# Optimization experiments

Measured on AMD Instinct MI355X. Metric: run time of the kernel, lower is better.

The kernel has to match this reference:

```python
import jax, jax.numpy as jnp
import numpy as np

DIM, H, W, DEPTH = 256, 64, 64, 4
D_STATE, DT_RANK, D_CONV = 8, 16, 4
G, AGENTS = 8, 4

PKEYS = ['ln_w','ln_b','in_proj_w','conv_w','conv_b','x_proj_w','dt_proj_w','dt_proj_b',
         'A_log','A_b_log','D','out_proj_w','mn_w','mn_b']


def layernorm(x, w, b, eps=1e-5):
    mu = jnp.mean(x, -1, keepdims=True)
    var = jnp.var(x, -1, keepdims=True)
    return (x - mu) * jax.lax.rsqrt(var + eps) * w + b


def causal_conv1d(x, w, b):
    # x: (g, d, L); w: (d, k) depthwise causal conv (pad left k-1)
    k = w.shape[-1]
    xp = jnp.pad(x, ((0, 0), (0, 0), (k - 1, 0)))
    y = jax.lax.conv_general_dilated(xp, w[:, None, :], (1,), 'VALID',
                                     dimension_numbers=('NCH', 'OIH', 'NCH'),
                                     feature_group_count=w.shape[0])
    return y + b[None, :, None]


def selective_scan(u, delta, A, B, C, Dp, z):
    # u, delta, z: (g, d, L); B, C: (g, n, L); A: (d, n); Dp: (d,)
    dT = jnp.moveaxis(delta, -1, 0)
    BT = jnp.moveaxis(B, -1, 0)
    CT = jnp.moveaxis(C, -1, 0)
    uT = jnp.moveaxis(u, -1, 0)
    h0 = jnp.zeros(u.shape[:2] + (A.shape[-1],), u.dtype)  # (g, d, n)

    def step(h, inp):
        d_t, B_t, C_t, u_t = inp  # (g,d),(g,n),(g,n),(g,d)
        h = jnp.exp(d_t[..., None] * A) * h + (d_t * u_t)[..., None] * B_t[:, None, :]
        return h, jnp.einsum('gdn,gn->gd', h, C_t)

    _, ys = jax.lax.scan(step, h0, (dT, BT, CT, uT))
    y = jnp.moveaxis(ys, 0, -1) + Dp[None, :, None] * u
    return y * jax.nn.silu(z)


def ssm_dir(xdl, zdl, p, A):
    # one scan direction of mamba_inner_fn_no_out_proj; xdl, zdl: (g, d, L)
    xc = jax.nn.silu(causal_conv1d(xdl, p['conv_w'], p['conv_b']))
    x_dbl = jnp.einsum('gdl,ed->gel', xc, p['x_proj_w'])  # e = dt_rank + 2n
    dt, B, C = jnp.split(x_dbl, [DT_RANK, DT_RANK + D_STATE], axis=1)
    delta = jax.nn.softplus(jnp.einsum('grl,dr->gdl', dt, p['dt_proj_w'])
                            + p['dt_proj_b'][None, :, None])
    return selective_scan(xc, delta, A, B, C, p['D'], zdl)


def single_mamba_block(x, p):
    # x: (g, L, c)  -- LayerNorm + bidirectional Mamba (bimamba v1) + residual
    skip = x
    xn = layernorm(x, p['ln_w'], p['ln_b'])
    xz = jnp.einsum('glc,ec->gle', xn, p['in_proj_w'])  # (g, L, 2d), no bias
    xx, z = jnp.split(xz, 2, axis=-1)
    xdl = jnp.swapaxes(xx, 1, 2)
    zdl = jnp.swapaxes(z, 1, 2)
    y_f = ssm_dir(xdl, zdl, p, -jnp.exp(p['A_log']))
    y_b = jnp.flip(ssm_dir(jnp.flip(xdl, -1), jnp.flip(zdl, -1), p, -jnp.exp(p['A_b_log'])), -1)
    y = 0.5 * (y_f + y_b)  # if_devide_out=True
    out = jnp.einsum('gdl,od->glo', y, p['out_proj_w'])  # no bias
    out = layernorm(out, p['mn_w'], p['mn_b'])  # use_norm=True
    return out + skip


def _forward(data, plist, record_len):
    b, c, h, w = data.shape
    rl = np.asarray(record_len)
    seg = jnp.asarray(np.repeat(np.arange(rl.shape[0]), rl))
    means = jax.ops.segment_sum(data, seg, num_segments=rl.shape[0]) \
        / jnp.asarray(rl, data.dtype)[:, None, None, None]
    x = means.reshape(rl.shape[0], c, h * w).transpose(0, 2, 1)  # (G, L, C)
    for i in range(DEPTH):
        p = {k: v[i] for k, v in zip(PKEYS, plist)}
        x = single_mamba_block(x, p)
    return x.transpose(0, 2, 1).reshape(rl.shape[0], c, h, w)


def setup_inputs() -> dict:
    key = jax.random.key(0)
    ks = jax.random.split(key, 8)
    nrm = lambda k, shape, sc: jax.random.normal(k, shape, jnp.float32) * sc
    Alog = jnp.zeros((DEPTH, DIM, D_STATE), jnp.float32) \
        + jnp.log(jnp.arange(1, D_STATE + 1, dtype=jnp.float32))
    return {
        'data': jax.random.normal(ks[0], (G * AGENTS, DIM, H, W), jnp.float32),
        'ln_w': jnp.ones((DEPTH, DIM)), 'ln_b': jnp.zeros((DEPTH, DIM)),
        'in_proj_w': nrm(ks[1], (DEPTH, 2 * DIM, DIM), 0.02),
        'conv_w': nrm(ks[2], (DEPTH, DIM, D_CONV), 0.3),
        'conv_b': jnp.zeros((DEPTH, DIM)),
        'x_proj_w': nrm(ks[3], (DEPTH, DT_RANK + 2 * D_STATE, DIM), 0.02),
        'dt_proj_w': nrm(ks[4], (DEPTH, DIM, DT_RANK), 0.1),
        'dt_proj_b': jnp.full((DEPTH, DIM), float(np.log(np.expm1(0.01))), jnp.float32),
        'A_log': Alog, 'A_b_log': Alog,
        'D': jnp.ones((DEPTH, DIM)),
        'out_proj_w': nrm(ks[5], (DEPTH, DIM, DIM), 0.02),
        'mn_w': jnp.ones((DEPTH, DIM)), 'mn_b': jnp.zeros((DEPTH, DIM)),
        'record_len': jnp.full((G,), AGENTS, dtype=jnp.int32),
    }


def reference(data, ln_w, ln_b, in_proj_w, conv_w, conv_b, x_proj_w, dt_proj_w, dt_proj_b,
              A_log, A_b_log, D, out_proj_w, mn_w, mn_b, record_len):
    plist = [ln_w, ln_b, in_proj_w, conv_w, conv_b, x_proj_w, dt_proj_w, dt_proj_b,
             A_log, A_b_log, D, out_proj_w, mn_w, mn_b]
    return _forward(data, plist, record_len)
```

## Files before the change

### kernel.cpp

```cpp
#include <hip/hip_runtime.h>
#include <hip/hip_bf16.h>
#include <cstdint>
#include <cstddef>

typedef unsigned short u16;
typedef unsigned int   u32;

typedef short s16x8 __attribute__((ext_vector_type(8)));
typedef float f32x4 __attribute__((ext_vector_type(4)));

__device__ __forceinline__ float b2f(u16 u){ u32 x = ((u32)u)<<16; float f; __builtin_memcpy(&f,&x,4); return f; }
__device__ __forceinline__ u16  f2b(float f){ u32 x; __builtin_memcpy(&x,&f,4); u32 r = x + 0x7FFFu + ((x>>16)&1u); return (u16)(r>>16); }

__device__ __forceinline__ void unpack8(uint4 v, float* o){
  o[0]=b2f((u16)v.x); o[1]=b2f((u16)(v.x>>16));
  o[2]=b2f((u16)v.y); o[3]=b2f((u16)(v.y>>16));
  o[4]=b2f((u16)v.z); o[5]=b2f((u16)(v.z>>16));
  o[6]=b2f((u16)v.w); o[7]=b2f((u16)(v.w>>16));
}

__device__ __forceinline__ void gl_lds16(const u16* g, u16* l){
  __builtin_amdgcn_global_load_lds((const __attribute__((address_space(1))) u32*)g,
                                   (__attribute__((address_space(3))) u32*)l, 16, 0, 0);
}

__global__ void k_detect(const u16* __restrict__ lnw, int* __restrict__ flag){
  if (threadIdx.x==0 && blockIdx.x==0) *flag = (lnw[0] == 0x3F80) ? 1 : 0;
}

struct CvtTable { const void* src[14]; u16* dst[14]; int n[14]; };
__global__ void k_cvt(CvtTable t, const int* __restrict__ flag){
  int ti = blockIdx.y;
  int n = t.n[ti];
  int isbf = *flag;
  const u16*  sb = (const u16*)t.src[ti];
  const float* sf = (const float*)t.src[ti];
  u16* d = t.dst[ti];
  for (int i = blockIdx.x*256 + threadIdx.x; i < n; i += gridDim.x*256)
    d[i] = isbf ? sb[i] : f2b(sf[i]);
}

__global__ void k_mean(const void* __restrict__ data, const int* __restrict__ rl,
                       float* __restrict__ x, const int* __restrict__ flag){
  __shared__ float tile[32][129];
  int isbf = *flag;
  const u16*  db = (const u16*)data;
  const float* df_ = (const float*)data;
  int g = blockIdx.z, c0 = blockIdx.y*32, l0 = blockIdx.x*128;
  int tid = threadIdx.x;
  int off=0; for(int i=0;i<g;i++) off += rl[i];
  int cnt = rl[g];
  float inv = 1.0f/(float)cnt;
  for(int it=0; it<16; ++it){
    int idx = it*256 + tid;
    int ci = idx>>7, lj = idx&127;
    float acc = 0.f;
    for(int b=0;b<cnt;b++){
      size_t gi = ((size_t)(off+b)*256 + (c0+ci)) * 4096 + (l0+lj);
      acc += isbf ? b2f(db[gi]) : df_[gi];
    }
    tile[ci][lj] = acc*inv;
  }
  __syncthreads();
  for(int it=0; it<16; ++it){
    int idx = it*256 + tid;
    int lj = idx>>5, ci = idx&31;
    x[ ((size_t)g*4096 + (l0+lj))*256 + (c0+ci) ] = tile[ci][lj];
  }
}

__global__ void k_prep(const u16* __restrict__ dtp, const u16* __restrict__ xpw, u16* __restrict__ bcomb){
  int layer = blockIdx.y, row = blockIdx.x, c = threadIdx.x;
  u16 out;
  if (row < 256){
    float acc = 0.f;
    #pragma unroll
    for(int r=0;r<16;r++)
      acc += b2f(dtp[(size_t)layer*4096 + row*16 + r]) * b2f(xpw[(size_t)layer*8192 + r*256 + c]);
    out = f2b(acc);
  } else if (row < 272){
    out = xpw[(size_t)layer*8192 + (16 + row - 256)*256 + c];
  } else {
    out = 0;
  }
  bcomb[((size_t)layer*384 + row)*256 + c] = out;
}

__global__ void k_ln1(const float* __restrict__ x, u16* __restrict__ xnh, u16* __restrict__ xnl,
                      const u16* __restrict__ w, const u16* __restrict__ b, int layer){
  int wid = threadIdx.x>>6, lane = threadIdx.x&63;
  int row = blockIdx.x*4 + wid;
  const float* xr = x + (size_t)row*256;
  float4 v = *(const float4*)(xr + lane*4);
  float s = v.x+v.y+v.z+v.w;
  float q = v.x*v.x+v.y*v.y+v.z*v.z+v.w*v.w;
  for(int o=32;o;o>>=1){ s += __shfl_xor(s,o); q += __shfl_xor(q,o); }
  float mu = s*(1.f/256.f);
  float var = q*(1.f/256.f) - mu*mu;
  float rs = rsqrtf(var + 1e-5f);
  const u16* wp = w + layer*256 + lane*4;
  const u16* bp = b + layer*256 + lane*4;
  float vv[4] = {v.x,v.y,v.z,v.w};
  u16 h4[4], l4[4];
  #pragma unroll
  for(int k2=0;k2<4;k2++){
    float xv = (vv[k2]-mu)*rs*b2f(wp[k2]) + b2f(bp[k2]);
    h4[k2] = f2b(xv);
    l4[k2] = f2b(xv - b2f(h4[k2]));
  }
  uint2 oh; oh.x = (u32)h4[0] | ((u32)h4[1]<<16); oh.y = (u32)h4[2] | ((u32)h4[3]<<16);
  uint2 ol; ol.x = (u32)l4[0] | ((u32)l4[1]<<16); ol.y = (u32)l4[2] | ((u32)l4[3]<<16);
  *(uint2*)(xnh + (size_t)row*256 + lane*4) = oh;
  *(uint2*)(xnl + (size_t)row*256 + lane*4) = ol;
}

template<int MODE>
__global__ __launch_bounds__(256)
void k_gemm(const u16* __restrict__ A, const u16* __restrict__ Alo,
            const u16* __restrict__ B,
            u16* __restrict__ C0, float* __restrict__ C0f, int ldC,
            const u16* __restrict__ bias, u16* __restrict__ C1){
  __shared__ u16 As[128*64];
  __shared__ u16 Bs[128*64];
  __shared__ u16 Asl[(MODE==0)?(128*64):16];
  int tid = threadIdx.x, wid = tid>>6, lane = tid&63;
  int m0 = blockIdx.x*128, n0 = blockIdx.y*128;
  f32x4 acc[4][4];
  #pragma unroll
  for(int i=0;i<4;i++)
    #pragma unroll
    for(int j=0;j<4;j++) acc[i][j] = (f32x4){0.f,0.f,0.f,0.f};
  int lrow  = lane>>3;
  int scol  = ((lane&7) ^ lrow) * 8;
  int rm = (wid&1)*64, cn = (wid>>1)*64;
  for(int k0=0;k0<256;k0+=64){
    #pragma unroll
    for(int it=0; it<4; ++it){
      int chunk = wid*4 + it;
      int row = chunk*8 + lrow;
      gl_lds16(A + (size_t)(m0+row)*256 + k0 + scol, As + chunk*512 + lane*8);
      if (MODE==0)
        gl_lds16(Alo + (size_t)(m0+row)*256 + k0 + scol, Asl + chunk*512 + lane*8);
      gl_lds16(B + (size_t)(n0+row)*256 + k0 + scol, Bs + chunk*512 + lane*8);
    }
    __syncthreads();
    #pragma unroll
    for(int kk=0;kk<2;kk++){
      s16x8 af[4], afl[4], bfr[4];
      #pragma unroll
      for(int i=0;i<4;i++){
        int ar = rm + i*16 + (lane&15);
        int ap = (kk*4 + (lane>>4)) ^ (ar&7);
        af[i]  = *(const s16x8*)(As + ar*64 + ap*8);
        if (MODE==0) afl[i] = *(const s16x8*)(Asl + ar*64 + ap*8);
        int br = cn + i*16 + (lane&15);
        int bp = (kk*4 + (lane>>4)) ^ (br&7);
        bfr[i] = *(const s16x8*)(Bs + br*64 + bp*8);
      }
      #pragma unroll
      for(int i=0;i<4;i++)
        #pragma unroll
        for(int j=0;j<4;j++){
          acc[i][j] = __builtin_amdgcn_mfma_f32_16x16x32_bf16(af[i], bfr[j], acc[i][j], 0,0,0);
          if (MODE==0)
            acc[i][j] = __builtin_amdgcn_mfma_f32_16x16x32_bf16(afl[i], bfr[j], acc[i][j], 0,0,0);
        }
    }
    __syncthreads();
  }
  #pragma unroll
  for(int i=0;i<4;i++){
    #pragma unroll
    for(int j=0;j<4;j++){
      int n  = n0 + cn + j*16 + (lane&15);
      int mB = m0 + rm + i*16 + ((lane>>4)<<2);
      #pragma unroll
      for(int r=0;r<4;r++){
        float val = acc[i][j][r];
        int m = mB + r;
        if (MODE==0){
          C0f[(size_t)m*ldC + n] = val;
        } else {
          if (n < 256){
            float v2 = val + b2f(bias[n]);
            float sp = (v2 > 15.f) ? v2 : __logf(1.f + __expf(v2));
            C0[(size_t)m*256 + n] = f2b(sp);
          } else if (n < 272){
            C1[(size_t)m*16 + (n-256)] = f2b(val);
          }
        }
      }
    }
  }
}

__global__ void k_conv(const float* __restrict__ xzf, const u16* __restrict__ cw,
                       const u16* __restrict__ cb, u16* __restrict__ xcf, u16* __restrict__ xcb_, int layer){
  int l0 = blockIdx.x*32, g = blockIdx.y, d = threadIdx.x;
  float w[4];
  #pragma unroll
  for(int j=0;j<4;j++) w[j] = b2f(cw[(size_t)layer*1024 + d*4 + j]);
  float bb = b2f(cb[layer*256 + d]);
  float xv[38];
  #pragma unroll
  for(int t=0;t<38;t++){
    int lp = l0 - 3 + t;
    xv[t] = (lp>=0 && lp<4096) ? xzf[((size_t)g*4096 + lp)*512 + d] : 0.f;
  }
  #pragma unroll
  for(int i=0;i<32;i++){
    float af = bb, ab = bb;
    #pragma unroll
    for(int j=0;j<4;j++){ af += w[j]*xv[i+j]; ab += w[j]*xv[i+6-j]; }
    af = af / (1.f + __expf(-af));
    ab = ab / (1.f + __expf(-ab));
    size_t o = ((size_t)g*4096 + (l0+i))*256 + d;
    xcf[o]  = f2b(af);
    xcb_[o] = f2b(ab);
  }
}

__global__ __launch_bounds__(256)
void k_scan1(const u16* __restrict__ df, const u16* __restrict__ db,
             const u16* __restrict__ uf, const u16* __restrict__ ub,
             const u16* __restrict__ bcf, const u16* __restrict__ bcb,
             const u16* __restrict__ Alog, const u16* __restrict__ Ablog,
             float* __restrict__ abuf, float* __restrict__ bbuf, int layer){
  int c = blockIdx.x, g = blockIdx.y, dir = blockIdx.z, d = threadIdx.x;
  const u16* dl = dir ? db : df;
  const u16* uu = dir ? ub : uf;
  const u16* bc = dir ? bcb : bcf;
  const u16* Al = dir ? Ablog : Alog;
  float An[8], h[8], ap[8];
  #pragma unroll
  for(int n=0;n<8;n++){
    An[n] = -__expf(b2f(Al[(size_t)layer*2048 + d*8 + n]));
    h[n] = 0.f; ap[n] = 1.f;
  }
  #pragma unroll 4
  for(int t=0;t<32;t++){
    int ts = c*32 + t;
    int tg = dir ? (4095 - ts) : ts;
    size_t rowo = (size_t)g*4096 + tg;
    float dv = b2f(dl[rowo*256 + d]);
    float uv = b2f(uu[rowo*256 + d]);
    uint4 bv = *(const uint4*)(bc + rowo*16);
    float bn[8]; unpack8(bv, bn);
    float du = dv*uv;
    #pragma unroll
    for(int n=0;n<8;n++){
      float da = __expf(dv*An[n]);
      h[n] = fmaf(da, h[n], du*bn[n]);
      ap[n] *= da;
    }
  }
  size_t base = ((((size_t)dir*8+g)*128 + c)*256 + d)*8;
  *(float4*)(abuf+base)   = (float4){ap[0],ap[1],ap[2],ap[3]};
  *(float4*)(abuf+base+4) = (float4){ap[4],ap[5],ap[6],ap[7]};
  *(float4*)(bbuf+base)   = (float4){h[0],h[1],h[2],h[3]};
  *(float4*)(bbuf+base+4) = (float4){h[4],h[5],h[6],h[7]};
}

__global__ void k_scan2(const float* __restrict__ abuf, const float* __restrict__ bbuf,
                        float* __restrict__ hs){
  int dblk = blockIdx.x, g = blockIdx.y, dir = blockIdx.z;
  int n = threadIdx.x & 7, dd = threadIdx.x >> 3;
  int d = dblk*8 + dd;
  float h = 0.f;
  size_t gofs = (((size_t)dir*8+g)*128);
  #pragma unroll 4
  for(int c=0;c<128;c++){
    size_t idx = ((gofs + c)*256 + d)*8 + n;
    hs[idx] = h;
    h = fmaf(abuf[idx], h, bbuf[idx]);
  }
}

__global__ __launch_bounds__(256)
void k_scanY(const u16* __restrict__ df, const u16* __restrict__ db,
             const float* __restrict__ xzf,
             const u16* __restrict__ bcf, const u16* __restrict__ bcb,
             const u16* __restrict__ Alog, const u16* __restrict__ Ablog,
             const u16* __restrict__ Dp, const u16* __restrict__ cw, const u16* __restrict__ cb,
             const float* __restrict__ hs,
             u16* __restrict__ yhi, u16* __restrict__ ylo, int layer){
  __shared__ float ybs[32*256];
  int c = blockIdx.x, g = blockIdx.y, d = threadIdx.x;
  int l0 = c*32;
  float Dd = b2f(Dp[layer*256 + d]);
  float w0 = b2f(cw[(size_t)layer*1024 + d*4 + 0]);
  float w1 = b2f(cw[(size_t)layer*1024 + d*4 + 1]);
  float w2 = b2f(cw[(size_t)layer*1024 + d*4 + 2]);
  float w3 = b2f(cw[(size_t)layer*1024 + d*4 + 3]);
  float cbb = b2f(cb[layer*256 + d]);
  const float* xrow = xzf + (size_t)g*4096*512 + d;
  const float* zrow = xrow + 256;
  float An[8], h[8];
  {
    #pragma unroll
    for(int n=0;n<8;n++) An[n] = -__expf(b2f(Ablog[(size_t)layer*2048 + d*8 + n]));
    size_t base = ((((size_t)8+g)*128 + (127-c))*256 + d)*8;
    float4 h0 = *(const float4*)(hs+base);
    float4 h1 = *(const float4*)(hs+base+4);
    h[0]=h0.x; h[1]=h0.y; h[2]=h0.z; h[3]=h0.w;
    h[4]=h1.x; h[5]=h1.y; h[6]=h1.z; h[7]=h1.w;
    float xw1 = (l0+32<4096) ? xrow[(size_t)(l0+32)*512] : 0.f;
    float xw2 = (l0+33<4096) ? xrow[(size_t)(l0+33)*512] : 0.f;
    float xw3 = (l0+34<4096) ? xrow[(size_t)(l0+34)*512] : 0.f;
    #pragma unroll 4
    for(int q=0;q<32;q++){
      int t = 31 - q;
      size_t rowo = (size_t)g*4096 + l0 + t;
      float x0 = xrow[(size_t)(l0+t)*512];
      float ucv = cbb + w3*x0 + w2*xw1 + w1*xw2 + w0*xw3;
      xw3 = xw2; xw2 = xw1; xw1 = x0;
      float uv = ucv / (1.f + __expf(-ucv));
      float dv = b2f(db[rowo*256 + d]);
      uint4 bv = *(const uint4*)(bcb + rowo*16);
      uint4 cv = *(const uint4*)(bcb + rowo*16 + 8);
      float bn[8], cn_[8];
      unpack8(bv, bn); unpack8(cv, cn_);
      float du = dv*uv;
      float y = 0.f;
      #pragma unroll
      for(int n=0;n<8;n++){
        float da = __expf(dv*An[n]);
        h[n] = fmaf(da, h[n], du*bn[n]);
        y = fmaf(h[n], cn_[n], y);
      }
      ybs[t*256 + d] = y + Dd*uv;
    }
  }
  {
    #pragma unroll
    for(int n=0;n<8;n++) An[n] = -__expf(b2f(Alog[(size_t)layer*2048 + d*8 + n]));
    size_t base = (((size_t)g*128 + c)*256 + d)*8;
    float4 h0 = *(const float4*)(hs+base);
    float4 h1 = *(const float4*)(hs+base+4);
    h[0]=h0.x; h[1]=h0.y; h[2]=h0.z; h[3]=h0.w;
    h[4]=h1.x; h[5]=h1.y; h[6]=h1.z; h[7]=h1.w;
    float wm1 = (l0-1>=0) ? xrow[(size_t)(l0-1)*512] : 0.f;
    float wm2 = (l0-2>=0) ? xrow[(size_t)(l0-2)*512] : 0.f;
    float wm3 = (l0-3>=0) ? xrow[(size_t)(l0-3)*512] : 0.f;
    #pragma unroll 4
    for(int t=0;t<32;t++){
      size_t rowo = (size_t)g*4096 + l0 + t;
      float x0 = xrow[(size_t)(l0+t)*512];
      float ucv = cbb + w0*wm3 + w1*wm2 + w2*wm1 + w3*x0;
      wm3 = wm2; wm2 = wm1; wm1 = x0;
      float uv = ucv / (1.f + __expf(-ucv));
      float dv = b2f(df[rowo*256 + d]);
      uint4 bv = *(const uint4*)(bcf + rowo*16);
      uint4 cv = *(const uint4*)(bcf + rowo*16 + 8);
      float bn[8], cn_[8];
      unpack8(bv, bn); unpack8(cv, cn_);
      float du = dv*uv;
      float y = 0.f;
      #pragma unroll
      for(int n=0;n<8;n++){
        float da = __expf(dv*An[n]);
        h[n] = fmaf(da, h[n], du*bn[n]);
        y = fmaf(h[n], cn_[n], y);
      }
      y += Dd*uv;
      y += ybs[t*256 + d];
      float zv = zrow[(size_t)(l0+t)*512];
      float yv = y * 0.5f * zv / (1.f + __expf(-zv));
      u16 hi = f2b(yv);
      yhi[rowo*256 + d] = hi;
      ylo[rowo*256 + d] = f2b(yv - b2f(hi));
    }
  }
}

template<int LAST>
__global__ __launch_bounds__(256)
void k_outproj(const u16* __restrict__ yhi, const u16* __restrict__ ylo,
               const u16* __restrict__ Bw,
               float* __restrict__ X, u16* __restrict__ xnh, u16* __restrict__ xnl,
               const u16* __restrict__ mnw, const u16* __restrict__ mnb,
               const u16* __restrict__ lnw_n, const u16* __restrict__ lnb_n){
  __shared__ u16 Ash[64*64];
  __shared__ u16 Asl[64*64];
  __shared__ u16 Bs[256*64];
  int tid = threadIdx.x, wid = tid>>6, lane = tid&63;
  int c = blockIdx.x, g = blockIdx.y;
  size_t row0 = (size_t)g*4096 + c*64;
  f32x4 acc[16];
  #pragma unroll
  for(int j=0;j<16;j++) acc[j] = (f32x4){0.f,0.f,0.f,0.f};
  int lrow = lane>>3;
  int scol = ((lane&7) ^ lrow) * 8;
  for(int k0=0;k0<256;k0+=64){
    #pragma unroll
    for(int it=0; it<2; ++it){
      int chunk = wid*2 + it;
      int row = chunk*8 + lrow;
      gl_lds16(yhi + (row0+row)*256 + k0 + scol, Ash + chunk*512 + lane*8);
      gl_lds16(ylo + (row0+row)*256 + k0 + scol, Asl + chunk*512 + lane*8);
    }
    #pragma unroll
    for(int it=0; it<8; ++it){
      int chunk = wid*8 + it;
      int row = chunk*8 + lrow;
      gl_lds16(Bw + (size_t)row*256 + k0 + scol, Bs + chunk*512 + lane*8);
    }
    __syncthreads();
    #pragma unroll
    for(int kk=0;kk<2;kk++){
      int ar = wid*16 + (lane&15);
      int q  = kk*4 + (lane>>4);
      s16x8 afh = *(const s16x8*)(Ash + ar*64 + (q^(ar&7))*8);
      s16x8 afl = *(const s16x8*)(Asl + ar*64 + (q^(ar&7))*8);
      #pragma unroll
      for(int j=0;j<16;j++){
        int br = j*16 + (lane&15);
        s16x8 bfv = *(const s16x8*)(Bs + br*64 + (q^(br&7))*8);
        acc[j] = __builtin_amdgcn_mfma_f32_16x16x32_bf16(afh, bfv, acc[j], 0,0,0);
        acc[j] = __builtin_amdgcn_mfma_f32_16x16x32_bf16(afl, bfv, acc[j], 0,0,0);
      }
    }
    __syncthreads();
  }
  size_t gm0 = row0;
  int quad = lane>>4;
  float sm[4]={0,0,0,0}, sq[4]={0,0,0,0};
  #pragma unroll
  for(int j=0;j<16;j++)
    #pragma unroll
    for(int r=0;r<4;r++){ float v=acc[j][r]; sm[r]+=v; sq[r]+=v*v; }
  #pragma unroll
  for(int o=1;o<16;o<<=1)
    #pragma unroll
    for(int r=0;r<4;r++){ sm[r]+=__shfl_xor(sm[r],o); sq[r]+=__shfl_xor(sq[r],o); }
  float mu[4], rs[4];
  #pragma unroll
  for(int r=0;r<4;r++){
    mu[r] = sm[r]*(1.f/256.f);
    float var = sq[r]*(1.f/256.f) - mu[r]*mu[r];
    rs[r] = rsqrtf(var + 1e-5f);
  }
  #pragma unroll
  for(int j=0;j<16;j++){
    int col = j*16 + (lane&15);
    float w = b2f(mnw[col]), bb = b2f(mnb[col]);
    #pragma unroll
    for(int r=0;r<4;r++){
      size_t m = gm0 + wid*16 + quad*4 + r;
      float xn = X[m*256 + col] + (acc[j][r]-mu[r])*rs[r]*w + bb;
      X[m*256 + col] = xn;
      acc[j][r] = xn;
    }
  }
  if (!LAST){
    float sm2[4]={0,0,0,0}, sq2[4]={0,0,0,0};
    #pragma unroll
    for(int j=0;j<16;j++)
      #pragma unroll
      for(int r=0;r<4;r++){ float v=acc[j][r]; sm2[r]+=v; sq2[r]+=v*v; }
    #pragma unroll
    for(int o=1;o<16;o<<=1)
      #pragma unroll
      for(int r=0;r<4;r++){ sm2[r]+=__shfl_xor(sm2[r],o); sq2[r]+=__shfl_xor(sq2[r],o); }
    float mu2[4], rs2[4];
    #pragma unroll
    for(int r=0;r<4;r++){
      mu2[r] = sm2[r]*(1.f/256.f);
      float var = sq2[r]*(1.f/256.f) - mu2[r]*mu2[r];
      rs2[r] = rsqrtf(var + 1e-5f);
    }
    #pragma unroll
    for(int j=0;j<16;j++){
      int col = j*16 + (lane&15);
      float w = b2f(lnw_n[col]), bb = b2f(lnb_n[col]);
      #pragma unroll
      for(int r=0;r<4;r++){
        size_t m = gm0 + wid*16 + quad*4 + r;
        float vv = (acc[j][r]-mu2[r])*rs2[r]*w + bb;
        u16 hi = f2b(vv);
        xnh[m*256 + col] = hi;
        xnl[m*256 + col] = f2b(vv - b2f(hi));
      }
    }
  }
}

__global__ void k_tr(const float* __restrict__ x, void* __restrict__ out, const int* __restrict__ flag){
  __shared__ float tile[32][129];
  int isbf = *flag;
  int l0 = blockIdx.x*128, c0 = blockIdx.y*32, g = blockIdx.z;
  int tid = threadIdx.x;
  for(int it=0; it<16; ++it){
    int idx = it*256 + tid;
    int lj = idx>>5, ci = idx&31;
    tile[ci][lj] = x[((size_t)g*4096 + l0+lj)*256 + c0+ci];
  }
  __syncthreads();
  for(int it=0; it<16; ++it){
    int idx = it*256 + tid;
    int lj = idx&127, ci = idx>>7;
    size_t o = ((size_t)g*256 + c0+ci)*4096 + l0+lj;
    float v = tile[ci][lj];
    if (isbf) ((u16*)out)[o] = f2b(v);
    else      ((float*)out)[o] = v;
  }
}

extern "C" void kernel_launch(void* const* d_in, const int* in_sizes, int n_in,
                              void* d_out, int out_size, void* d_ws, size_t ws_size,
                              hipStream_t stream){
  (void)in_sizes; (void)n_in; (void)out_size; (void)ws_size;
  const int* rl = (const int*)d_in[15];

  char* ws = (char*)d_ws;
  float* X    = (float*)(ws);
  float* XZf  = (float*)(ws + 33554432);
  u16*  XNl   = (u16*) (ws + 100663296);
  u16*  XCF   = (u16*) (ws + 117440512);
  u16*  XCB   = (u16*) (ws + 134217728);
  u16*  DF    = (u16*) (ws + 150994944);
  u16*  DB    = (u16*) (ws + 167772160);
  u16*  BCF   = (u16*) (ws + 184549376);
  u16*  BCB   = (u16*) (ws + 185597952);
  u16*  BCOMB = (u16*) (ws + 186646528);
  float* ABUF = (float*)(ws + 187432960);
  u16*  XNh   = (u16*) (ws + 187432960);
  float* BBUF = (float*)(ws + 204210176);
  float* HS   = (float*)(ws + 220987392);
  u16*  WCVT  = (u16*) (ws + 237764608);
  int*  FLAG  = (int*) (ws + 239493120);

  u16* YHI = XCF;
  u16* YLO = XCB;

  u16* W_lnw  = WCVT + 0;
  u16* W_lnb  = WCVT + 1024;
  u16* W_inp  = WCVT + 2048;
  u16* W_cw   = WCVT + 526336;
  u16* W_cb   = WCVT + 530432;
  u16* W_xp   = WCVT + 531456;
  u16* W_dtw  = WCVT + 564224;
  u16* W_dtb  = WCVT + 580608;
  u16* W_Al   = WCVT + 581632;
  u16* W_Abl  = WCVT + 589824;
  u16* W_D    = WCVT + 598016;
  u16* W_outp = WCVT + 599040;
  u16* W_mnw  = WCVT + 861184;
  u16* W_mnb  = WCVT + 862208;

  k_detect<<<1,64,0,stream>>>((const u16*)d_in[1], FLAG);

  CvtTable t;
  const int idxs[14] = {1,2,3,4,5,6,7,8,9,10,11,12,13,14};
  u16* dsts[14] = {W_lnw,W_lnb,W_inp,W_cw,W_cb,W_xp,W_dtw,W_dtb,W_Al,W_Abl,W_D,W_outp,W_mnw,W_mnb};
  const int ns[14] = {1024,1024,524288,4096,1024,32768,16384,1024,8192,8192,1024,262144,1024,1024};
  for(int i=0;i<14;i++){ t.src[i]=d_in[idxs[i]]; t.dst[i]=dsts[i]; t.n[i]=ns[i]; }
  k_cvt<<<dim3(32,14),256,0,stream>>>(t, FLAG);

  k_mean<<<dim3(32,8,8),256,0,stream>>>(d_in[0], rl, X, FLAG);
  k_prep<<<dim3(384,4),256,0,stream>>>(W_dtw, W_xp, BCOMB);
  k_ln1<<<8192,256,0,stream>>>(X, XNh, XNl, W_lnw, W_lnb, 0);

  for(int layer=0; layer<4; ++layer){
    k_gemm<0><<<dim3(256,4),256,0,stream>>>(XNh, XNl, W_inp + (size_t)layer*512*256,
                                            nullptr, XZf, 512, nullptr, nullptr);
    k_conv<<<dim3(128,8),256,0,stream>>>(XZf, W_cw, W_cb, XCF, XCB, layer);
    k_gemm<1><<<dim3(512,3),256,0,stream>>>(XCF, nullptr, BCOMB + (size_t)layer*384*256,
                                            DF, nullptr, 256, W_dtb + layer*256, BCF);
    k_scan1<<<dim3(128,8,2),256,0,stream>>>(DF,DB,XCF,XCB,BCF,BCB,W_Al,W_Abl,ABUF,BBUF,layer);
    k_scan2<<<dim3(32,8,2),64,0,stream>>>(ABUF,BBUF,HS);
    k_scanY<<<dim3(128,8),256,0,stream>>>(DF,DB,XZf,BCF,BCB,W_Al,W_Abl,W_D,W_cw,W_cb,HS,YHI,YLO,layer);
    if (layer < 3){
      k_outproj<0><<<dim3(64,8),256,0,stream>>>(YHI, YLO, W_outp + (size_t)layer*256*256,
                                                X, XNh, XNl,
                                                W_mnw + layer*256, W_mnb + layer*256,
                                                W_lnw + (layer+1)*256, W_lnb + (layer+1)*256);
    } else {
      k_outproj<1><<<dim3(64,8),256,0,stream>>>(YHI, YLO, W_outp + (size_t)layer*256*256,
                                                X, XNh, XNl,
                                                W_mnw + layer*256, W_mnb + layer*256,
                                                W_lnw, W_lnb);
    }
  }
  k_tr<<<dim3(32,8,8),256,0,stream>>>(X, d_out, FLAG);
}
```

Baseline: 1.271 ms.

## Store z gate as bf16 separately and drop hi/lo split of scan output

The in-projection GEMM now writes the x half as fp32 into a compact 256-wide buffer and the z half as bf16 into its own buffer. The conv and scan kernels read these narrower layouts. The scan output is stored only as a single bf16 value instead of a hi/lo bf16 pair, so the out-projection loads half the A tile and runs half as many MFMAs. This cuts memory traffic and matrix work, at the cost of lower precision in z and in the out-projection input.

Result: no change. 1.274 ms (+0.2%).

```diff
diff --git a/kernel.cpp b/kernel.cpp
--- a/kernel.cpp
+++ b/kernel.cpp
@@ -179,7 +179,8 @@
         float val = acc[i][j][r];
         int m = mB + r;
         if (MODE==0){
-          C0f[(size_t)m*ldC + n] = val;
+          if (n < 256) C0f[(size_t)m*256 + n] = val;
+          else         C1[(size_t)m*256 + (n-256)] = f2b(val);
         } else {
           if (n < 256){
             float v2 = val + b2f(bias[n]);
@@ -194,7 +195,7 @@
   }
 }
 
-__global__ void k_conv(const float* __restrict__ xzf, const u16* __restrict__ cw,
+__global__ void k_conv(const float* __restrict__ xf, const u16* __restrict__ cw,
                        const u16* __restrict__ cb, u16* __restrict__ xcf, u16* __restrict__ xcb_, int layer){
   int l0 = blockIdx.x*32, g = blockIdx.y, d = threadIdx.x;
   float w[4];
@@ -205,7 +206,7 @@
   #pragma unroll
   for(int t=0;t<38;t++){
     int lp = l0 - 3 + t;
-    xv[t] = (lp>=0 && lp<4096) ? xzf[((size_t)g*4096 + lp)*512 + d] : 0.f;
+    xv[t] = (lp>=0 && lp<4096) ? xf[((size_t)g*4096 + lp)*256 + d] : 0.f;
   }
   #pragma unroll
   for(int i=0;i<32;i++){
@@ -278,12 +279,12 @@
 
 __global__ __launch_bounds__(256)
 void k_scanY(const u16* __restrict__ df, const u16* __restrict__ db,
-             const float* __restrict__ xzf,
+             const float* __restrict__ xf, const u16* __restrict__ zb,
              const u16* __restrict__ bcf, const u16* __restrict__ bcb,
              const u16* __restrict__ Alog, const u16* __restrict__ Ablog,
              const u16* __restrict__ Dp, const u16* __restrict__ cw, const u16* __restrict__ cb,
              const float* __restrict__ hs,
-             u16* __restrict__ yhi, u16* __restrict__ ylo, int layer){
+             u16* __restrict__ yhi, int layer){
   __shared__ float ybs[32*256];
   int c = blockIdx.x, g = blockIdx.y, d = threadIdx.x;
   int l0 = c*32;
@@ -293,8 +294,8 @@
   float w2 = b2f(cw[(size_t)layer*1024 + d*4 + 2]);
   float w3 = b2f(cw[(size_t)layer*1024 + d*4 + 3]);
   float cbb = b2f(cb[layer*256 + d]);
-  const float* xrow = xzf + (size_t)g*4096*512 + d;
-  const float* zrow = xrow + 256;
+  const float* xrow = xf + (size_t)g*4096*256 + d;
+  const u16*  zrow = zb + (size_t)g*4096*256 + d;
   float An[8], h[8];
   {
     #pragma unroll
@@ -304,14 +305,14 @@
     float4 h1 = *(const float4*)(hs+base+4);
     h[0]=h0.x; h[1]=h0.y; h[2]=h0.z; h[3]=h0.w;
     h[4]=h1.x; h[5]=h1.y; h[6]=h1.z; h[7]=h1.w;
-    float xw1 = (l0+32<4096) ? xrow[(size_t)(l0+32)*512] : 0.f;
-    float xw2 = (l0+33<4096) ? xrow[(size_t)(l0+33)*512] : 0.f;
-    float xw3 = (l0+34<4096) ? xrow[(size_t)(l0+34)*512] : 0.f;
+    float xw1 = (l0+32<4096) ? xrow[(size_t)(l0+32)*256] : 0.f;
+    float xw2 = (l0+33<4096) ? xrow[(size_t)(l0+33)*256] : 0.f;
+    float xw3 = (l0+34<4096) ? xrow[(size_t)(l0+34)*256] : 0.f;
     #pragma unroll 4
     for(int q=0;q<32;q++){
       int t = 31 - q;
       size_t rowo = (size_t)g*4096 + l0 + t;
-      float x0 = xrow[(size_t)(l0+t)*512];
+      float x0 = xrow[(size_t)(l0+t)*256];
       float ucv = cbb + w3*x0 + w2*xw1 + w1*xw2 + w0*xw3;
       xw3 = xw2; xw2 = xw1; xw1 = x0;
       float uv = ucv / (1.f + __expf(-ucv));
@@ -339,13 +340,13 @@
     float4 h1 = *(const float4*)(hs+base+4);
     h[0]=h0.x; h[1]=h0.y; h[2]=h0.z; h[3]=h0.w;
     h[4]=h1.x; h[5]=h1.y; h[6]=h1.z; h[7]=h1.w;
-    float wm1 = (l0-1>=0) ? xrow[(size_t)(l0-1)*512] : 0.f;
-    float wm2 = (l0-2>=0) ? xrow[(size_t)(l0-2)*512] : 0.f;
-    float wm3 = (l0-3>=0) ? xrow[(size_t)(l0-3)*512] : 0.f;
+    float wm1 = (l0-1>=0) ? xrow[(size_t)(l0-1)*256] : 0.f;
+    float wm2 = (l0-2>=0) ? xrow[(size_t)(l0-2)*256] : 0.f;
+    float wm3 = (l0-3>=0) ? xrow[(size_t)(l0-3)*256] : 0.f;
     #pragma unroll 4
     for(int t=0;t<32;t++){
       size_t rowo = (size_t)g*4096 + l0 + t;
-      float x0 = xrow[(size_t)(l0+t)*512];
+      float x0 = xrow[(size_t)(l0+t)*256];
       float ucv = cbb + w0*wm3 + w1*wm2 + w2*wm1 + w3*x0;
       wm3 = wm2; wm2 = wm1; wm1 = x0;
       float uv = ucv / (1.f + __expf(-ucv));
@@ -364,24 +365,21 @@
       }
       y += Dd*uv;
       y += ybs[t*256 + d];
-      float zv = zrow[(size_t)(l0+t)*512];
+      float zv = b2f(zrow[(size_t)(l0+t)*256]);
       float yv = y * 0.5f * zv / (1.f + __expf(-zv));
-      u16 hi = f2b(yv);
-      yhi[rowo*256 + d] = hi;
-      ylo[rowo*256 + d] = f2b(yv - b2f(hi));
+      yhi[rowo*256 + d] = f2b(yv);
     }
   }
 }
 
 template<int LAST>
 __global__ __launch_bounds__(256)
-void k_outproj(const u16* __restrict__ yhi, const u16* __restrict__ ylo,
+void k_outproj(const u16* __restrict__ yhi,
                const u16* __restrict__ Bw,
                float* __restrict__ X, u16* __restrict__ xnh, u16* __restrict__ xnl,
                const u16* __restrict__ mnw, const u16* __restrict__ mnb,
                const u16* __restrict__ lnw_n, const u16* __restrict__ lnb_n){
   __shared__ u16 Ash[64*64];
-  __shared__ u16 Asl[64*64];
   __shared__ u16 Bs[256*64];
   int tid = threadIdx.x, wid = tid>>6, lane = tid&63;
   int c = blockIdx.x, g = blockIdx.y;
@@ -397,7 +395,6 @@
       int chunk = wid*2 + it;
       int row = chunk*8 + lrow;
       gl_lds16(yhi + (row0+row)*256 + k0 + scol, Ash + chunk*512 + lane*8);
-      gl_lds16(ylo + (row0+row)*256 + k0 + scol, Asl + chunk*512 + lane*8);
     }
     #pragma unroll
     for(int it=0; it<8; ++it){
@@ -411,13 +408,11 @@
       int ar = wid*16 + (lane&15);
       int q  = kk*4 + (lane>>4);
       s16x8 afh = *(const s16x8*)(Ash + ar*64 + (q^(ar&7))*8);
-      s16x8 afl = *(const s16x8*)(Asl + ar*64 + (q^(ar&7))*8);
       #pragma unroll
       for(int j=0;j<16;j++){
         int br = j*16 + (lane&15);
         s16x8 bfv = *(const s16x8*)(Bs + br*64 + (q^(br&7))*8);
         acc[j] = __builtin_amdgcn_mfma_f32_16x16x32_bf16(afh, bfv, acc[j], 0,0,0);
-        acc[j] = __builtin_amdgcn_mfma_f32_16x16x32_bf16(afl, bfv, acc[j], 0,0,0);
       }
     }
     __syncthreads();
@@ -515,23 +510,23 @@
   char* ws = (char*)d_ws;
   float* X    = (float*)(ws);
   float* XZf  = (float*)(ws + 33554432);
-  u16*  XNl   = (u16*) (ws + 100663296);
-  u16*  XCF   = (u16*) (ws + 117440512);
-  u16*  XCB   = (u16*) (ws + 134217728);
-  u16*  DF    = (u16*) (ws + 150994944);
-  u16*  DB    = (u16*) (ws + 167772160);
-  u16*  BCF   = (u16*) (ws + 184549376);
-  u16*  BCB   = (u16*) (ws + 185597952);
-  u16*  BCOMB = (u16*) (ws + 186646528);
-  float* ABUF = (float*)(ws + 187432960);
-  u16*  XNh   = (u16*) (ws + 187432960);
-  float* BBUF = (float*)(ws + 204210176);
-  float* HS   = (float*)(ws + 220987392);
-  u16*  WCVT  = (u16*) (ws + 237764608);
-  int*  FLAG  = (int*) (ws + 239493120);
+  u16*  ZB    = (u16*) (ws + 67108864);
+  u16*  XNl   = (u16*) (ws + 83886080);
+  u16*  XCF   = (u16*) (ws + 100663296);
+  u16*  XCB   = (u16*) (ws + 117440512);
+  u16*  DF    = (u16*) (ws + 134217728);
+  u16*  DB    = (u16*) (ws + 150994944);
+  u16*  BCF   = (u16*) (ws + 167772160);
+  u16*  BCB   = (u16*) (ws + 168820736);
+  u16*  BCOMB = (u16*) (ws + 169869312);
+  float* ABUF = (float*)(ws + 170655744);
+  u16*  XNh   = (u16*) (ws + 170655744);
+  float* BBUF = (float*)(ws + 187432960);
+  float* HS   = (float*)(ws + 204210176);
+  u16*  WCVT  = (u16*) (ws + 220987392);
+  int*  FLAG  = (int*) (ws + 222715904);
 
   u16* YHI = XCF;
-  u16* YLO = XCB;
 
   u16* W_lnw  = WCVT + 0;
   u16* W_lnb  = WCVT + 1024;
@@ -563,20 +558,20 @@
 
   for(int layer=0; layer<4; ++layer){
     k_gemm<0><<<dim3(256,4),256,0,stream>>>(XNh, XNl, W_inp + (size_t)layer*512*256,
-                                            nullptr, XZf, 512, nullptr, nullptr);
+                                            nullptr, XZf, 256, nullptr, ZB);
     k_conv<<<dim3(128,8),256,0,stream>>>(XZf, W_cw, W_cb, XCF, XCB, layer);
     k_gemm<1><<<dim3(512,3),256,0,stream>>>(XCF, nullptr, BCOMB + (size_t)layer*384*256,
                                             DF, nullptr, 256, W_dtb + layer*256, BCF);
     k_scan1<<<dim3(128,8,2),256,0,stream>>>(DF,DB,XCF,XCB,BCF,BCB,W_Al,W_Abl,ABUF,BBUF,layer);
     k_scan2<<<dim3(32,8,2),64,0,stream>>>(ABUF,BBUF,HS);
-    k_scanY<<<dim3(128,8),256,0,stream>>>(DF,DB,XZf,BCF,BCB,W_Al,W_Abl,W_D,W_cw,W_cb,HS,YHI,YLO,layer);
+    k_scanY<<<dim3(128,8),256,0,stream>>>(DF,DB,XZf,ZB,BCF,BCB,W_Al,W_Abl,W_D,W_cw,W_cb,HS,YHI,layer);
     if (layer < 3){
-      k_outproj<0><<<dim3(64,8),256,0,stream>>>(YHI, YLO, W_outp + (size_t)layer*256*256,
+      k_outproj<0><<<dim3(64,8),256,0,stream>>>(YHI, W_outp + (size_t)layer*256*256,
                                                 X, XNh, XNl,
                                                 W_mnw + layer*256, W_mnb + layer*256,
                                                 W_lnw + (layer+1)*256, W_lnb + (layer+1)*256);
     } else {
-      k_outproj<1><<<dim3(64,8),256,0,stream>>>(YHI, YLO, W_outp + (size_t)layer*256*256,
+      k_outproj<1><<<dim3(64,8),256,0,stream>>>(YHI, W_outp + (size_t)layer*256*256,
                                                 X, XNh, XNl,
                                                 W_mnw + layer*256, W_mnb + layer*256,
                                                 W_lnw, W_lnb);
```
